# Performance work log

Hardware: AMD Instinct MI355X
Metric: run time of the kernel (lower is better)

## Reference

```python
import jax, jax.numpy as jnp
import numpy as np

D = 64        # gat_output_dim == state_dim
HID = 128     # hidden_dim
ADIM = 2 * D  # action_dim (ope_dim + insert_dim)


def _mk(key, shape, scale=0.05):
    return jax.random.normal(key, shape, dtype=jnp.float32) * scale


def setup_inputs() -> dict:
    key = jax.random.key(0)
    ks = jax.random.split(key, 24)
    inp = {
        "ope_gat": jax.random.normal(ks[0], (8, 258, D), jnp.float32),
        "insert_gat": jax.random.normal(ks[1], (8, 256, D), jnp.float32),
        "h": jax.random.normal(ks[2], (8, D), jnp.float32),
        "c": jax.random.normal(ks[3], (8, D), jnp.float32),
        # LSTM (pytorch layout: gates i,f,g,o stacked -> [4D, in])
        "W_ih": _mk(ks[4], (4 * D, D)),
        "W_hh": _mk(ks[5], (4 * D, D)),
        "b_ih": _mk(ks[6], (4 * D,)),
        "b_hh": _mk(ks[7], (4 * D,)),
        # V_net: Linear(D,HID) -> Linear(HID,HID) -> LeakyReLU -> Linear(HID,1)
        "Wv0": _mk(ks[8], (HID, D)), "bv0": _mk(ks[9], (HID,)),
        "Wv1": _mk(ks[10], (HID, HID)), "bv1": _mk(ks[11], (HID,)),
        "Wv2": _mk(ks[12], (1, HID)), "bv2": _mk(ks[13], (1,)),
        # A_net: Linear(D+ADIM,HID) -> Linear(HID,HID) -> LeakyReLU -> Linear(HID,1)
        "Wa0": _mk(ks[14], (HID, D + ADIM)), "ba0": _mk(ks[15], (HID,)),
        "Wa1": _mk(ks[16], (HID, HID)), "ba1": _mk(ks[17], (HID,)),
        "Wa2": _mk(ks[18], (1, HID)), "ba2": _mk(ks[19], (1,)),
    }
    return inp


def _lrelu(x):
    return jnp.where(x >= 0, x, 0.01 * x)


def _forward(ope_gat, insert_gat, h, c,
             W_ih, W_hh, b_ih, b_hh,
             Wv0, bv0, Wv1, bv1, Wv2, bv2,
             Wa0, ba0, Wa1, ba1, Wa2, ba2):
    ope = ope_gat[:, 1:-1]                # [B, O, D]
    state = ope.mean(axis=-2)             # [B, D]

    # single-step LSTM (pytorch gate order i, f, g, o)
    gates = state @ W_ih.T + b_ih + h @ W_hh.T + b_hh  # [B, 4D]
    i_g, f_g, g_g, o_g = jnp.split(gates, 4, axis=-1)
    cn = jax.nn.sigmoid(f_g) * c + jax.nn.sigmoid(i_g) * jnp.tanh(g_g)
    hn = jax.nn.sigmoid(o_g) * jnp.tanh(cn)
    rnn_state = hn                        # [B, D]

    # V head (note: no activation after first linear -- name-overwrite bug)
    V = _lrelu((rnn_state @ Wv0.T + bv0) @ Wv1.T + bv1) @ Wv2.T + bv2  # [B, 1]

    # A head on the full (ope x insert) cross-join; ope side is detached.
    ope_d = jax.lax.stop_gradient(ope)    # [B, O, D]
    B, O, _ = ope_d.shape
    I = insert_gat.shape[1]
    # Decompose first linear over the concat [state | ope | insert] (exact math).
    Ws, Wo, Wi = Wa0[:, :D], Wa0[:, D:2 * D], Wa0[:, 2 * D:]
    h0 = (rnn_state @ Ws.T)[:, None, None, :] \
         + jnp.einsum('bod,hd->boh', ope_d, Wo)[:, :, None, :] \
         + jnp.einsum('bid,hd->bih', insert_gat, Wi)[:, None, :, :] \
         + ba0                              # [B, O, I, HID]
    h1 = _lrelu(jnp.einsum('boih,gh->boig', h0, Wa1) + ba1)
    A = (jnp.einsum('boih,h->boi', h1, Wa2[0]) + ba2[0]).reshape(B, O * I)
    return V, A, hn, cn


def reference(ope_gat, insert_gat, h, c,
              W_ih, W_hh, b_ih, b_hh,
              Wv0, bv0, Wv1, bv1, Wv2, bv2,
              Wa0, ba0, Wa1, ba1, Wa2, ba2):
    return _forward(ope_gat, insert_gat, h, c,
                    W_ih, W_hh, b_ih, b_hh,
                    Wv0, bv0, Wv1, bv1, Wv2, bv2,
                    Wa0, ba0, Wa1, ba1, Wa2, ba2)
```

## Files before the change

kernel.cpp:

```cpp
#include <hip/hip_runtime.h>
#include <hip/hip_bf16.h>
#include <math.h>

typedef unsigned short u16;


__device__ __forceinline__ u16 f2b(float x) { __hip_bfloat16 b = __float2bfloat16(x); return *(u16*)&b; }
__device__ __forceinline__ void cvt8(const uint4 u, float* f) {
    f[0] = __uint_as_float(u.x << 16); f[1] = __uint_as_float(u.x & 0xFFFF0000u);
    f[2] = __uint_as_float(u.y << 16); f[3] = __uint_as_float(u.y & 0xFFFF0000u);
    f[4] = __uint_as_float(u.z << 16); f[5] = __uint_as_float(u.z & 0xFFFF0000u);
    f[6] = __uint_as_float(u.w << 16); f[7] = __uint_as_float(u.w & 0xFFFF0000u);
}

__global__ __launch_bounds__(256) void k1_head(
    const float* __restrict__ ope, const float* __restrict__ hin, const float* __restrict__ cin,
    const float* __restrict__ W_ih, const float* __restrict__ W_hh,
    const float* __restrict__ b_ih, const float* __restrict__ b_hh,
    const float* __restrict__ Wv0, const float* __restrict__ bv0,
    const float* __restrict__ Wv1, const float* __restrict__ bv1,
    const float* __restrict__ Wv2, const float* __restrict__ bv2,
    const float* __restrict__ Wa0, const float* __restrict__ ba0,
    const float* __restrict__ Wa2, const float* __restrict__ ba2,
    float* __restrict__ ws, int fb)
{
    const int b = blockIdx.x, t = threadIdx.x;
    __shared__ float red[256], state[64], hvec[64], gl[256], hn_s[64], t0a[128], t1a[128];

    {
        const int d = t & 63, q = t >> 6;
        const float* p = ope + b * 16512 + (1 + q * 64) * 64 + d;
        float s = 0.f;
        #pragma unroll 8
        for (int r = 0; r < 64; ++r) s += p[r * 64];
        red[t] = s;
    }
    __syncthreads();
    if (t < 64)       state[t]   = (red[t] + red[t+64] + red[t+128] + red[t+192]) * (1.f/256.f);
    else if (t < 128) hvec[t-64] = hin[b*64 + (t-64)];
    __syncthreads();

    {
        float g = b_ih[t] + b_hh[t];
        #pragma unroll 8
        for (int d = 0; d < 64; ++d)
            g += state[d] * W_ih[t*64 + d] + hvec[d] * W_hh[t*64 + d];
        gl[t] = g;
    }
    __syncthreads();

    if (t < 64) {
        const float ig = gl[t], fg = gl[64+t], gg = gl[128+t], og = gl[192+t];
        const float c  = cin[b*64 + t];
        const float si = 1.f/(1.f + expf(-ig));
        const float sf = 1.f/(1.f + expf(-fg));
        const float so = 1.f/(1.f + expf(-og));
        const float cn = sf*c + si*tanhf(gg);
        const float hn = so*tanhf(cn);
        ws[fb + 1288 + b*64 + t] = hn;
        ws[fb + 1800 + b*64 + t] = cn;
        hn_s[t] = hn;
    }
    __syncthreads();

    if (t < 128) {
        float a = bv0[t];
        #pragma unroll 8
        for (int d = 0; d < 64; ++d) a += hn_s[d] * Wv0[t*64 + d];
        t0a[t] = a;
    }
    __syncthreads();
    if (t < 128) {
        float a = bv1[t];
        #pragma unroll 8
        for (int d = 0; d < 128; ++d) a += t0a[d] * Wv1[t*128 + d];
        a = (a >= 0.f) ? a : 0.01f*a;
        t1a[t] = a * Wv2[t];
        float s2 = ba0[t];
        #pragma unroll 8
        for (int d = 0; d < 64; ++d) s2 += hn_s[d] * Wa0[t*192 + d];
        ws[fb + b*128 + t] = s2;
        const float w2v = Wa2[t];
        ws[fb + 1024 + t] = w2v;
        ws[fb + 1152 + t] = -0.99f * w2v;
    }
    __syncthreads();
    if (t == 0) {
        float v = bv2[0];
        for (int g = 0; g < 128; ++g) v += t1a[g];
        ws[fb + 1280 + b] = v;
        ws[fb + 2313]    = ba2[0];
    }
}

template<bool MF32>
__device__ void k2_body(const float* ope, const float* ins, const float* Wa0,
    const float* Wa1, const float* ba1, float* ws, int fb,
    u16* Wa1s, u16* Wsel, u16* inrows, float* P)
{
    const int t = threadIdx.x;
    const int b = blockIdx.x >> 5;
    const int r0 = (blockIdx.x & 31) * 16;
    const int side = (r0 >= 256) ? 1 : 0;

    #pragma unroll
    for (int k = 0; k < 16; ++k) {
        const int e4 = t + k*256;
        const int g = e4 >> 5, hq = (e4 & 31) * 4;
        const float4 w = *(const float4*)(Wa1 + g*128 + hq);
        ushort4 u; u.x = f2b(w.x); u.y = f2b(w.y); u.z = f2b(w.z); u.w = f2b(w.w);
        *(ushort4*)&Wa1s[g*136 + hq] = u;
    }
    #pragma unroll
    for (int k = 0; k < 8; ++k) {
        const int e4 = t + k*256;
        const int h = e4 >> 4, dq = (e4 & 15) * 4;
        const float4 w = *(const float4*)(Wa0 + h*192 + 64 + side*64 + dq);
        ushort4 u; u.x = f2b(w.x); u.y = f2b(w.y); u.z = f2b(w.z); u.w = f2b(w.w);
        *(ushort4*)&Wsel[h*72 + dq] = u;
    }
    {
        const int r = t >> 4, dq = (t & 15) * 4;
        const float* src = side
            ? (ins + b*16384 + (r0 - 256 + r)*64 + dq)
            : (ope + b*16512 + (1 + r0 + r)*64 + dq);
        const float4 w = *(const float4*)src;
        ushort4 u; u.x = f2b(w.x); u.y = f2b(w.y); u.z = f2b(w.z); u.w = f2b(w.w);
        *(ushort4*)&inrows[r*72 + dq] = u;
    }
    __syncthreads();

    const int r = t >> 4;
    const int q = t & 15;

    {
        float acc[8];
        #pragma unroll
        for (int k = 0; k < 8; ++k)
            acc[k] = side ? 0.0f : ws[fb + b*128 + (q + 16*k)];
        #pragma unroll
        for (int d8 = 0; d8 < 64; d8 += 8) {
            float iv[8];
            cvt8(*(const uint4*)&inrows[r*72 + d8], iv);
            #pragma unroll
            for (int k = 0; k < 8; ++k) {
                float wv[8];
                cvt8(*(const uint4*)&Wsel[(q + 16*k)*72 + d8], wv);
                #pragma unroll
                for (int j = 0; j < 8; ++j) acc[k] += wv[j] * iv[j];
            }
        }
        #pragma unroll
        for (int k = 0; k < 8; ++k) P[r*132 + q + 16*k] = acc[k];
    }
    __syncthreads();

    {
        float acc[8] = {0.f,0.f,0.f,0.f,0.f,0.f,0.f,0.f};
        #pragma unroll
        for (int h8 = 0; h8 < 128; h8 += 8) {
            const float4 p0 = *(const float4*)&P[r*132 + h8];
            const float4 p1 = *(const float4*)&P[r*132 + h8 + 4];
            #pragma unroll
            for (int k = 0; k < 8; ++k) {
                float wv[8];
                cvt8(*(const uint4*)&Wa1s[(q + 16*k)*136 + h8], wv);
                float a = acc[k];
                a += wv[0]*p0.x + wv[1]*p0.y + wv[2]*p0.z + wv[3]*p0.w;
                a += wv[4]*p1.x + wv[5]*p1.y + wv[6]*p1.z + wv[7]*p1.w;
                acc[k] = a;
            }
        }
        if (!side) {
            const int row = b*256 + r0 + r;
            #pragma unroll
            for (int k = 0; k < 8; ++k) {
                const int g = q + 16*k;
                const float v = acc[k] + ba1[g];
                if (MF32) ws[row*128 + g] = v;
                else      ((u16*)ws)[row*128 + g] = f2b(v);
            }
        } else {
            const int row = b*256 + (r0 - 256) + r;
            #pragma unroll
            for (int k = 0; k < 8; ++k) {
                const int g = q + 16*k;
                if (MF32) ws[262144 + row*128 + g] = acc[k];
                else      ((u16*)ws)[262144 + row*128 + g] = f2b(acc[k]);
            }
        }
    }
}

__global__ __launch_bounds__(256) void k2_xy(
    const float* ope, const float* ins, const float* Wa0, const float* Wa1,
    const float* ba1, float* ws, int fb, int mf32)
{
    __shared__ __align__(16) u16 Wa1s[128*136];
    __shared__ __align__(16) u16 Wsel[128*72];
    __shared__ __align__(16) u16 inrows[16*72];
    __shared__ __align__(16) float P[16*132];
    if (mf32) k2_body<true >(ope, ins, Wa0, Wa1, ba1, ws, fb, Wa1s, Wsel, inrows, P);
    else      k2_body<false>(ope, ins, Wa0, Wa1, ba1, ws, fb, Wa1s, Wsel, inrows, P);
}

template<bool MF32>
__device__ void k3_body(const float* ws, float* out, int fb)
{
    const int t = threadIdx.x;
    const int b = blockIdx.x >> 6;
    const int o0 = (blockIdx.x & 63) * 4;
    const float* w2  = ws + fb + 1024;
    const float* w2n = ws + fb + 1152;

    float y[128];
    if (MF32) {
        const float* yr = ws + 262144 + (b*256 + t)*128;
        #pragma unroll
        for (int k = 0; k < 32; ++k) *(float4*)&y[k*4] = *(const float4*)(yr + k*4);
    } else {
        const u16* yr = (const u16*)ws + 262144 + (b*256 + t)*128;
        #pragma unroll
        for (int k = 0; k < 16; ++k) cvt8(*(const uint4*)(yr + k*8), &y[k*8]);
    }

    float acc[4] = {0.f, 0.f, 0.f, 0.f};
    #pragma unroll
    for (int gc = 0; gc < 16; ++gc) {
        float wa[8], wb[8];
        { const float4 a0 = *(const float4*)(w2  + gc*8);
          const float4 a1 = *(const float4*)(w2  + gc*8 + 4);
          wa[0]=a0.x; wa[1]=a0.y; wa[2]=a0.z; wa[3]=a0.w;
          wa[4]=a1.x; wa[5]=a1.y; wa[6]=a1.z; wa[7]=a1.w; }
        { const float4 b0 = *(const float4*)(w2n + gc*8);
          const float4 b1 = *(const float4*)(w2n + gc*8 + 4);
          wb[0]=b0.x; wb[1]=b0.y; wb[2]=b0.z; wb[3]=b0.w;
          wb[4]=b1.x; wb[5]=b1.y; wb[6]=b1.z; wb[7]=b1.w; }
        #pragma unroll
        for (int o = 0; o < 4; ++o) {
            float xv[8];
            if (MF32) {
                const float* xr = ws + (b*256 + o0 + o)*128 + gc*8;
                const float4 x0 = *(const float4*)xr;
                const float4 x1 = *(const float4*)(xr + 4);
                xv[0]=x0.x; xv[1]=x0.y; xv[2]=x0.z; xv[3]=x0.w;
                xv[4]=x1.x; xv[5]=x1.y; xv[6]=x1.z; xv[7]=x1.w;
            } else {
                const u16* xr = (const u16*)ws + (b*256 + o0 + o)*128 + gc*8;
                cvt8(*(const uint4*)xr, xv);
            }
            float a = acc[o];
            #pragma unroll
            for (int j = 0; j < 8; ++j) {
                const float v = xv[j] + y[gc*8 + j];
                const float m = fminf(v, 0.f);
                a = fmaf(wa[j], v, fmaf(wb[j], m, a));
            }
            acc[o] = a;
        }
    }
    const float ba2 = ws[fb + 2313];
    #pragma unroll
    for (int o = 0; o < 4; ++o)
        out[8 + b*65536 + (o0 + o)*256 + t] = acc[o] + ba2;

    if (blockIdx.x == 0) {
        if (t < 8) out[t] = ws[fb + 1280 + t];
        #pragma unroll
        for (int j = t; j < 512; j += 256) {
            out[524296 + j] = ws[fb + 1288 + j];
            out[524808 + j] = ws[fb + 1800 + j];
        }
    }
}

__global__ __launch_bounds__(256, 2) void k3_adv(const float* ws, float* out,
                                                 int fb, int mf32)
{
    if (mf32) k3_body<true >(ws, out, fb);
    else      k3_body<false>(ws, out, fb);
}

extern "C" void kernel_launch(void* const* d_in, const int* in_sizes, int n_in,
                              void* d_out, int out_size, void* d_ws, size_t ws_size,
                              hipStream_t stream) {
    float* ws = (float*)d_ws;
    float* out = (float*)d_out;
    const int mf32 = (ws_size >= (size_t)2200000) ? 1 : 0;
    const int fb   = mf32 ? 524288 : 262144;

    const float* ope = (const float*)d_in[0];
    const float* ins = (const float*)d_in[1];

    k1_head<<<dim3(8),   dim3(256), 0, stream>>>(
        ope, (const float*)d_in[2], (const float*)d_in[3],
        (const float*)d_in[4], (const float*)d_in[5],
        (const float*)d_in[6], (const float*)d_in[7],
        (const float*)d_in[8], (const float*)d_in[9],
        (const float*)d_in[10], (const float*)d_in[11],
        (const float*)d_in[12], (const float*)d_in[13],
        (const float*)d_in[14], (const float*)d_in[15],
        (const float*)d_in[18], (const float*)d_in[19], ws, fb);
    k2_xy  <<<dim3(256), dim3(256), 0, stream>>>(
        ope, ins, (const float*)d_in[14], (const float*)d_in[16],
        (const float*)d_in[17], ws, fb, mf32);
    k3_adv <<<dim3(512), dim3(256), 0, stream>>>(ws, out, fb, mf32);
}
```

Measured before the change: 136.8 us.

## Rewrite leaky-ReLU dot as linear term plus abs term, precomputing linear parts

Uses lrelu(v)=0.505v+0.495|v| so the linear part of the final dot product separates over the ope and insert rows. Those per-row partial sums are computed in k2 with wave shuffles and stored in the workspace. k3 then only accumulates the |x+y| term. k3 also streams y in chunks of 16 instead of holding 128 floats in registers, and the occupancy hint of 2 on its launch bounds is dropped. This removes the fmin and one FMA per element and lowers register pressure. The cost is extra workspace writes and reduction work in k2.

```diff
diff --git a/kernel.cpp b/kernel.cpp
--- a/kernel.cpp
+++ b/kernel.cpp
@@ -81,8 +81,8 @@
         for (int d = 0; d < 64; ++d) s2 += hn_s[d] * Wa0[t*192 + d];
         ws[fb + b*128 + t] = s2;
         const float w2v = Wa2[t];
-        ws[fb + 1024 + t] = w2v;
-        ws[fb + 1152 + t] = -0.99f * w2v;
+        ws[fb + 1024 + t] = 0.505f * w2v;
+        ws[fb + 1152 + t] = 0.495f * w2v;
     }
     __syncthreads();
     if (t == 0) {
@@ -171,12 +171,14 @@
                 acc[k] = a;
             }
         }
+        float part = 0.f;
         if (!side) {
             const int row = b*256 + r0 + r;
             #pragma unroll
             for (int k = 0; k < 8; ++k) {
                 const int g = q + 16*k;
                 const float v = acc[k] + ba1[g];
+                part = fmaf(ws[fb + 1024 + g], v, part);
                 if (MF32) ws[row*128 + g] = v;
                 else      ((u16*)ws)[row*128 + g] = f2b(v);
             }
@@ -185,9 +187,18 @@
             #pragma unroll
             for (int k = 0; k < 8; ++k) {
                 const int g = q + 16*k;
+                part = fmaf(ws[fb + 1024 + g], acc[k], part);
                 if (MF32) ws[262144 + row*128 + g] = acc[k];
                 else      ((u16*)ws)[262144 + row*128 + g] = f2b(acc[k]);
             }
+        }
+        part += __shfl_xor(part, 1);
+        part += __shfl_xor(part, 2);
+        part += __shfl_xor(part, 4);
+        part += __shfl_xor(part, 8);
+        if (q == 0) {
+            if (!side) ws[fb + 2320 + b*256 + r0 + r] = part + ws[fb + 2313];
+            else       ws[fb + 4368 + b*256 + (r0 - 256) + r] = part;
         }
     }
 }
@@ -210,59 +221,46 @@
     const int t = threadIdx.x;
     const int b = blockIdx.x >> 6;
     const int o0 = (blockIdx.x & 63) * 4;
-    const float* w2  = ws + fb + 1024;
-    const float* w2n = ws + fb + 1152;
-
-    float y[128];
-    if (MF32) {
-        const float* yr = ws + 262144 + (b*256 + t)*128;
-        #pragma unroll
-        for (int k = 0; k < 32; ++k) *(float4*)&y[k*4] = *(const float4*)(yr + k*4);
-    } else {
-        const u16* yr = (const u16*)ws + 262144 + (b*256 + t)*128;
-        #pragma unroll
-        for (int k = 0; k < 16; ++k) cvt8(*(const uint4*)(yr + k*8), &y[k*8]);
-    }
+    const float* wb = ws + fb + 1152;
 
     float acc[4] = {0.f, 0.f, 0.f, 0.f};
     #pragma unroll
-    for (int gc = 0; gc < 16; ++gc) {
-        float wa[8], wb[8];
-        { const float4 a0 = *(const float4*)(w2  + gc*8);
-          const float4 a1 = *(const float4*)(w2  + gc*8 + 4);
-          wa[0]=a0.x; wa[1]=a0.y; wa[2]=a0.z; wa[3]=a0.w;
-          wa[4]=a1.x; wa[5]=a1.y; wa[6]=a1.z; wa[7]=a1.w; }
-        { const float4 b0 = *(const float4*)(w2n + gc*8);
-          const float4 b1 = *(const float4*)(w2n + gc*8 + 4);
-          wb[0]=b0.x; wb[1]=b0.y; wb[2]=b0.z; wb[3]=b0.w;
-          wb[4]=b1.x; wb[5]=b1.y; wb[6]=b1.z; wb[7]=b1.w; }
+    for (int gc = 0; gc < 8; ++gc) {
+        float yv[16], wv[16];
+        if (MF32) {
+            const float* yr = ws + 262144 + (b*256 + t)*128 + gc*16;
+            #pragma unroll
+            for (int k = 0; k < 4; ++k) *(float4*)&yv[k*4] = *(const float4*)(yr + k*4);
+        } else {
+            const u16* yr = (const u16*)ws + 262144 + (b*256 + t)*128 + gc*16;
+            cvt8(*(const uint4*)yr, yv);
+            cvt8(*(const uint4*)(yr + 8), yv + 8);
+        }
+        #pragma unroll
+        for (int k = 0; k < 4; ++k) *(float4*)&wv[k*4] = *(const float4*)(wb + gc*16 + k*4);
         #pragma unroll
         for (int o = 0; o < 4; ++o) {
-            float xv[8];
+            float xv[16];
             if (MF32) {
-                const float* xr = ws + (b*256 + o0 + o)*128 + gc*8;
-                const float4 x0 = *(const float4*)xr;
-                const float4 x1 = *(const float4*)(xr + 4);
-                xv[0]=x0.x; xv[1]=x0.y; xv[2]=x0.z; xv[3]=x0.w;
-                xv[4]=x1.x; xv[5]=x1.y; xv[6]=x1.z; xv[7]=x1.w;
+                const float* xr = ws + (b*256 + o0 + o)*128 + gc*16;
+                #pragma unroll
+                for (int k = 0; k < 4; ++k) *(float4*)&xv[k*4] = *(const float4*)(xr + k*4);
             } else {
-                const u16* xr = (const u16*)ws + (b*256 + o0 + o)*128 + gc*8;
+                const u16* xr = (const u16*)ws + (b*256 + o0 + o)*128 + gc*16;
                 cvt8(*(const uint4*)xr, xv);
+                cvt8(*(const uint4*)(xr + 8), xv + 8);
             }
             float a = acc[o];
             #pragma unroll
-            for (int j = 0; j < 8; ++j) {
-                const float v = xv[j] + y[gc*8 + j];
-                const float m = fminf(v, 0.f);
-                a = fmaf(wa[j], v, fmaf(wb[j], m, a));
-            }
+            for (int j = 0; j < 16; ++j)
+                a = fmaf(wv[j], fabsf(xv[j] + yv[j]), a);
             acc[o] = a;
         }
     }
-    const float ba2 = ws[fb + 2313];
+    const float c2 = ws[fb + 4368 + b*256 + t];
     #pragma unroll
     for (int o = 0; o < 4; ++o)
-        out[8 + b*65536 + (o0 + o)*256 + t] = acc[o] + ba2;
+        out[8 + b*65536 + (o0 + o)*256 + t] = ws[fb + 2320 + b*256 + o0 + o] + c2 + acc[o];
 
     if (blockIdx.x == 0) {
         if (t < 8) out[t] = ws[fb + 1280 + t];
@@ -274,8 +272,8 @@
     }
 }
 
-__global__ __launch_bounds__(256, 2) void k3_adv(const float* ws, float* out,
-                                                 int fb, int mf32)
+__global__ __launch_bounds__(256) void k3_adv(const float* ws, float* out,
+                                              int fb, int mf32)
 {
     if (mf32) k3_body<true >(ws, out, fb);
     else      k3_body<false>(ws, out, fb);
```

Measured after the change: 133.8 us. 2.2% less time.
